# Performance work log

Hardware: AMD Instinct MI355X
Metric: run time of the kernel (lower is better)

Reference implementation:

```python
import jax, jax.numpy as jnp
import numpy as np

B, T, W, H, F = 256, 128, 32, 512, 1024


def setup_inputs() -> dict:
    key = jax.random.key(0)
    ks = jax.random.split(key, 8)
    s = 0.05
    return {
        "inputs": jax.random.normal(ks[0], (B, T, 2), jnp.float32),
        "Wk": jax.random.normal(ks[1], (2, 4 * H), jnp.float32) * s,
        "Wr": jax.random.normal(ks[2], (H, 4 * H), jnp.float32) * s,
        "b": jnp.zeros((4 * H,), jnp.float32),
        "Ww": jax.random.normal(ks[3], (H, 2), jnp.float32) * s,
        "bw": jnp.zeros((2,), jnp.float32),
        "Wc": jax.random.normal(ks[4], (2, H), jnp.float32) * s,
        "bc": jnp.zeros((H,), jnp.float32),
        "Wcc": jax.random.normal(ks[5], (W * H, F), jnp.float32) * s,
        "bcc": jnp.zeros((F,), jnp.float32),
        "Wp": jax.random.normal(ks[6], (F, 2), jnp.float32) * s,
        "bp": jnp.zeros((2,), jnp.float32),
        "Wco": jax.random.normal(ks[7], (F, 1), jnp.float32) * s,
        "bco": jnp.zeros((1,), jnp.float32),
    }


def _cell(x, h, c, Wk, Wr, b):
    # Keras LSTMCell: gate order i, f, g(candidate), o; sigmoid recurrent act, tanh act.
    z = x @ Wk + h @ Wr + b
    i, f, g, o = jnp.split(z, 4, axis=-1)
    c = jax.nn.sigmoid(f) * c + jax.nn.sigmoid(i) * jnp.tanh(g)
    h = jax.nn.sigmoid(o) * jnp.tanh(c)
    return h, c


def reference(inputs, Wk, Wr, b, Ww, bw, Wc, bc, Wcc, bcc, Wp, bp, Wco, bco):
    # Masking(-1.0) is a no-op for Gaussian inputs; dropout is identity at inference.
    warm_seq = jnp.swapaxes(inputs[:, W:], 0, 1)  # [T-W, B, 2]
    h0 = jnp.zeros((inputs.shape[0], H), inputs.dtype)
    c0 = jnp.zeros_like(h0)

    def warm_step(carry, x):
        h, c = carry
        h, c = _cell(x, h, c, Wk, Wr, b)
        return (h, c), None

    (h, c), _ = jax.lax.scan(warm_step, (h0, c0), warm_seq)
    warm_out = h  # warm_up_lstm_output, [B, H]
    pred0 = h @ Ww + bw  # dense_warm (linear activation), [B, 2]

    def dec_step(carry, _):
        h, c, pred = carry
        h, c = _cell(pred, h, c, Wk, Wr, b)
        pred = h @ Ww + bw
        return (h, c, pred), pred

    n_dec = T - W - 1  # range(1, time - warm_up_length)
    _, preds_rest = jax.lax.scan(dec_step, (h, c, pred0), None, length=n_dec)
    predictions = jnp.concatenate([pred0[None], preds_rest], axis=0)  # [T-W, B, 2]
    predictions = jnp.swapaxes(predictions, 0, 1)  # [B, T-W, 2]

    cand = jax.nn.relu(inputs[:, : W - 1] @ Wc + bc)  # [B, W-1, H]
    cand = cand.reshape(cand.shape[0], -1)  # flatten -> [B, (W-1)*H]
    cat = jnp.concatenate([warm_out, cand], axis=1)  # [B, W*H]
    ct = jax.nn.relu(cat @ Wcc + bcc)  # dense_concat, [B, F]
    candidate_prob = jax.nn.sigmoid(ct @ Wp + bp)  # [B, 2]
    candidate_cost = ct @ Wco + bco  # [B, 1]
    return predictions, candidate_cost, candidate_prob, inputs
```

## Files before the change

### kernel.cpp

```cpp
#include <hip/hip_runtime.h>
#include <hip/hip_bf16.h>
#include <stdint.h>

#define B_    256
#define T_    128
#define W_    32
#define H_    512
#define G4_   2048
#define TW_   96
#define STEPS_ 191
#define TEAMS 16
#define MEMBERS 16
#define ROWS  16
#define HC    32

typedef __attribute__((ext_vector_type(8))) short short8;
typedef __attribute__((ext_vector_type(4))) float f32x4;
typedef __attribute__((ext_vector_type(4))) uint32_t u32x4;

__device__ __forceinline__ unsigned short f2bf(float f) {
  uint32_t u = __float_as_uint(f);
  u += 0x7fffu + ((u >> 16) & 1u);
  return (unsigned short)(u >> 16);
}
__device__ __forceinline__ float sigm(float x) { return 1.f / (1.f + __expf(-x)); }
__device__ __forceinline__ float tanh_(float x) { return 1.f - 2.f / (1.f + __expf(2.f * x)); }

#define LOAD_CF(p)      __hip_atomic_load((p), __ATOMIC_RELAXED, __HIP_MEMORY_SCOPE_AGENT)
#define LOAD_CI(p)      __hip_atomic_load((p), __ATOMIC_RELAXED, __HIP_MEMORY_SCOPE_AGENT)
#define ARRIVE(p)       __hip_atomic_fetch_add((p), 1, __ATOMIC_RELAXED, __HIP_MEMORY_SCOPE_AGENT)

__device__ __forceinline__ u32x4 ld16c(const void* p) {
  u32x4 v;
  asm volatile("global_load_dwordx4 %0, %1, off sc0 sc1"
               : "=&v"(v) : "v"(p) : "memory");
  return v;
}
__device__ __forceinline__ void st16c(void* p, u32x4 v) {
  asm volatile("global_store_dwordx4 %0, %1, off sc0 sc1" :: "v"(p), "v"(v) : "memory");
}
__device__ __forceinline__ void stf16c(void* p, f32x4 v) {
  asm volatile("global_store_dwordx4 %0, %1, off sc0 sc1" :: "v"(p), "v"(v) : "memory");
}

__global__ __launch_bounds__(256, 1) void lstm_kernel(
    const float* __restrict__ inputs, const float* __restrict__ Wk,
    const float* __restrict__ Wr, const float* __restrict__ bias,
    const float* __restrict__ Ww, const float* __restrict__ bw,
    unsigned short* __restrict__ h0buf, unsigned short* __restrict__ h1buf,
    float* __restrict__ pp0, float* __restrict__ pp1,
    unsigned short* __restrict__ warm, int* __restrict__ flags,
    float* __restrict__ out_pred)
{
  const int team = blockIdx.x & 15;
  const int member = blockIdx.x >> 4;
  const int rbase = team * ROWS;
  const int hbase = member * HC;
  const int tid = threadIdx.x;
  const int wave = tid >> 6;
  const int lane = tid & 63;
  const int l4 = lane >> 4, l16 = lane & 15;

  __shared__ unsigned short h_lds[ROWS][H_];
  __shared__ float x_all[TW_][ROWS][2];
  __shared__ float x_lds[ROWS][2];
  __shared__ float pp_lds[4][ROWS][2];
  __shared__ alignas(16) unsigned short h_out[ROWS][HC];

  for (int i = tid; i < TW_*ROWS*2; i += 256) {
    int tt = i >> 5, row = (i >> 1) & 15, c = i & 1;
    x_all[tt][row][c] = inputs[(size_t)(rbase+row)*(T_*2) + (W_+tt)*2 + c];
  }

  const int gateL = l16 & 3, hclL = l16 >> 2;
  short8 afrag[2][16];
  float bbv[2][4], wk0v[2][4], wk1v[2][4], wwv[2][2];
#pragma unroll
  for (int a = 0; a < 2; a++) {
    const int gcA = gateL*H_ + hbase + wave*8 + a*4 + hclL;
#pragma unroll
    for (int ks = 0; ks < 16; ks++) {
      const float* wp = Wr + (size_t)(ks*32 + l4*8) * G4_ + gcA;
#pragma unroll
      for (int j = 0; j < 8; j++) afrag[a][ks][j] = (short)f2bf(wp[(size_t)j * G4_]);
    }
    const int colA = hbase + wave*8 + a*4 + l4;
#pragma unroll
    for (int j = 0; j < 4; j++) {
      int gcj = j*H_ + colA;
      bbv[a][j] = bias[gcj]; wk0v[a][j] = Wk[gcj]; wk1v[a][j] = Wk[G4_ + gcj];
    }
    wwv[a][0] = Ww[2*colA]; wwv[a][1] = Ww[2*colA + 1];
  }
  const float bwc0 = bw[0], bwc1 = bw[1];
  float creg[2] = {0.f, 0.f};
  __syncthreads();

  int* ctr = flags + team * 16;
  const int srow = tid >> 4, sg = tid & 15;

  for (int t = 0; t < STEPS_; t++) {
    const unsigned short* hprev = (t & 1) ? h1buf : h0buf;
    unsigned short* hnext = (t & 1) ? h0buf : h1buf;
    const float* ppprev = (t & 1) ? pp1 : pp0;
    float* ppnext = (t & 1) ? pp0 : pp1;

    const bool dox = (t >= TW_) && (tid < 32);
    float vals[MEMBERS];
    if (dox) {
      int row = tid >> 1, c = tid & 1;
      const float* pps = ppprev + (size_t)team*MEMBERS*32 + row*2 + c;
#pragma unroll
      for (int m = 0; m < MEMBERS; m++) vals[m] = LOAD_CF(pps + m*32);
    }
    u32x4 q[4];
    {
      const unsigned short* srcb = hprev + (size_t)(rbase+srow)*H_ + sg*8;
#pragma unroll
      for (int i = 0; i < 4; i++) q[i] = ld16c(srcb + i*128);
    }
    asm volatile("s_waitcnt vmcnt(0)" ::: "memory");
    __builtin_amdgcn_sched_barrier(0);
#pragma unroll
    for (int i = 0; i < 4; i++)
      *(u32x4*)&h_lds[srow][((sg + 16*i) ^ (srow & 7)) * 8] = q[i];
    if (dox) {
      int row = tid >> 1, c = tid & 1;
      float s = c ? bwc1 : bwc0;
#pragma unroll
      for (int m = 0; m < MEMBERS; m++) s += vals[m];
      x_lds[row][c] = s;
      if (member == 0)
        out_pred[((size_t)(rbase+row)*96 + (t - TW_))*2 + c] = s;
    }
    __syncthreads();

    f32x4 acc[2];
    const float* xsrc = (t < TW_) ? &x_all[t][0][0] : &x_lds[0][0];
    {
      float x0 = xsrc[2*l16], x1 = xsrc[2*l16 + 1];
#pragma unroll
      for (int a = 0; a < 2; a++)
#pragma unroll
        for (int j = 0; j < 4; j++)
          acc[a][j] = bbv[a][j] + wk0v[a][j]*x0 + wk1v[a][j]*x1;
    }
#pragma unroll
    for (int ks = 0; ks < 16; ks++) {
      int pg = ((ks*4 + l4) ^ (l16 & 7)) * 8;
      short8 b0 = *(const short8*)&h_lds[l16][pg];
      acc[0] = __builtin_amdgcn_mfma_f32_16x16x32_bf16(afrag[0][ks], b0, acc[0], 0,0,0);
      acc[1] = __builtin_amdgcn_mfma_f32_16x16x32_bf16(afrag[1][ks], b0, acc[1], 0,0,0);
    }

    float pp0v = 0.f, pp1v = 0.f;
#pragma unroll
    for (int a = 0; a < 2; a++) {
      float zi = acc[a][0], zf = acc[a][1], zg = acc[a][2], zo = acc[a][3];
      float cn = sigm(zf)*creg[a] + sigm(zi)*tanh_(zg);
      float hn = sigm(zo)*tanh_(cn);
      creg[a] = cn;
      pp0v += hn * wwv[a][0];
      pp1v += hn * wwv[a][1];
      h_out[l16][wave*8 + a*4 + l4] = f2bf(hn);
    }
    if (t >= TW_ - 1) {
      pp0v += __shfl_xor(pp0v, 16); pp0v += __shfl_xor(pp0v, 32);
      pp1v += __shfl_xor(pp1v, 16); pp1v += __shfl_xor(pp1v, 32);
      if (l4 == 0) {
        pp_lds[wave][l16][0] = pp0v;
        pp_lds[wave][l16][1] = pp1v;
      }
    }
    __syncthreads();

    if (tid < 64) {
      int row = tid >> 2, qd = tid & 3;
      u32x4 v = *(const u32x4*)&h_out[row][qd*8];
      st16c(hnext + (size_t)(rbase+row)*H_ + hbase + qd*8, v);
      if (t == TW_ - 1)
        *(u32x4*)(warm + (size_t)(rbase+row)*H_ + hbase + qd*8) = v;
    }
    if (t >= TW_ - 1 && tid < 8) {
      f32x4 pv;
#pragma unroll
      for (int j = 0; j < 4; j++) {
        int idx = tid*4 + j, row = idx >> 1, c = idx & 1;
        pv[j] = pp_lds[0][row][c] + pp_lds[1][row][c]
              + pp_lds[2][row][c] + pp_lds[3][row][c];
      }
      stf16c(ppnext + (size_t)(team*MEMBERS + member)*32 + tid*4, pv);
    }

    asm volatile("s_waitcnt vmcnt(0)" ::: "memory");
    __syncthreads();
    if (tid == 0) {
      ARRIVE(ctr);
      int need = MEMBERS * (t + 1);
      while (LOAD_CI(ctr) < need) {}
    }
    __syncthreads();
  }

  if (member == 0 && tid < 32) {
    int row = tid >> 1, c = tid & 1;
    const float* pps = pp1 + (size_t)team*MEMBERS*32 + row*2 + c;
    float s = c ? bwc1 : bwc0;
#pragma unroll
    for (int m = 0; m < MEMBERS; m++) s += LOAD_CF(pps + m*32);
    out_pred[((size_t)(rbase+row)*96 + 95)*2 + c] = s;
  }
}

__global__ __launch_bounds__(256, 1) void gemm_kernel(
    const float* __restrict__ inputs, const float* __restrict__ Wc,
    const float* __restrict__ bc, const float* __restrict__ Wcc,
    float* __restrict__ partialT)
{
  __shared__ float wc0[512], wc1[512], bcl[512];
  __shared__ float xin[256][10];

  const int tid = threadIdx.x;
  const int wave = tid >> 6, lane = tid & 63;
  const int l4 = lane >> 4, l16 = lane & 15;
  const int nc = blockIdx.x & 31, kc = blockIdx.x >> 5;
  const int koff = (kc == 0) ? 0 : kc*2048 - 512;
  const int nks  = (kc == 0) ? 48 : 64;
  const int w0 = koff >> 9;
  const int nw = (kc == 0) ? 3 : 5;

  for (int i = tid; i < 512; i += 256) {
    wc0[i] = Wc[i]; wc1[i] = Wc[512 + i]; bcl[i] = bc[i];
  }
  for (int i = tid; i < 256*nw*2; i += 256) {
    int row = i / (nw*2), r = i - row*(nw*2);
    xin[row][r] = inputs[(size_t)row*(T_*2) + w0*2 + r];
  }
  __syncthreads();

  const int nhalf = wave & 1, bhalf = wave >> 1;
  const int nrow = nc*32 + nhalf*16 + l16;
  f32x4 zero = {0.f,0.f,0.f,0.f};
  f32x4 acc[8];
#pragma unroll
  for (int i = 0; i < 8; i++) acc[i] = zero;

  for (int ks = 0; ks < nks; ks++) {
    const int kkl = koff + ks*32 + l4*8;
    const float* wp = Wcc + (size_t)(512 + kkl) * 1024 + nrow;
    short8 af;
#pragma unroll
    for (int j = 0; j < 8; j++) af[j] = (short)f2bf(wp[(size_t)j * 1024]);
    const int w = kkl >> 9, hc = kkl & 511;
    const int wi = (w - w0)*2;
    float c0[8], c1[8], cb[8];
#pragma unroll
    for (int j = 0; j < 8; j++) {
      c0[j] = wc0[hc+j]; c1[j] = wc1[hc+j]; cb[j] = bcl[hc+j];
    }
#pragma unroll
    for (int bt = 0; bt < 8; bt++) {
      int row = bhalf*128 + bt*16 + l16;
      float x0 = xin[row][wi], x1 = xin[row][wi+1];
      short8 bf;
#pragma unroll
      for (int j = 0; j < 8; j++) {
        float v = fmaf(x0, c0[j], fmaf(x1, c1[j], cb[j]));
        bf[j] = (short)f2bf(fmaxf(v, 0.f));
      }
      acc[bt] = __builtin_amdgcn_mfma_f32_16x16x32_bf16(af, bf, acc[bt], 0,0,0);
    }
  }
  float* pp = partialT + (size_t)kc*262144
            + (size_t)(nc*32 + nhalf*16 + l4*4)*256 + bhalf*128 + l16;
#pragma unroll
  for (int bt = 0; bt < 8; bt++)
#pragma unroll
    for (int r = 0; r < 4; r++)
      pp[(size_t)r*256 + bt*16] = acc[bt][r];
}

__global__ __launch_bounds__(256, 1) void gemm0_kernel(
    const unsigned short* __restrict__ warm, const float* __restrict__ Wcc,
    float* __restrict__ partial8)
{
  const int nc = blockIdx.x;
  const int tid = threadIdx.x;
  const int w = tid >> 6, lane = tid & 63;
  const int l4 = lane >> 4, l16 = lane & 15;

  f32x4 zero = {0.f,0.f,0.f,0.f};
  f32x4 acc[16];
#pragma unroll
  for (int i = 0; i < 16; i++) acc[i] = zero;

  const int nrow = nc*64 + w*16 + l16;
  for (int ks = 0; ks < 16; ks++) {
    const float* wp = Wcc + (size_t)(ks*32 + l4*8) * 1024 + nrow;
    short8 af;
#pragma unroll
    for (int j = 0; j < 8; j++) af[j] = (short)f2bf(wp[(size_t)j * 1024]);
    const unsigned short* cp = warm + ks*32 + l4*8;
#pragma unroll
    for (int bt = 0; bt < 16; bt++) {
      short8 bf = *(const short8*)(cp + (size_t)(bt*16 + l16) * 512);
      acc[bt] = __builtin_amdgcn_mfma_f32_16x16x32_bf16(af, bf, acc[bt], 0,0,0);
    }
  }
  float* pp = partial8 + (size_t)(nc*64 + w*16 + l4*4)*256 + l16;
#pragma unroll
  for (int bt = 0; bt < 16; bt++)
#pragma unroll
    for (int r = 0; r < 4; r++)
      pp[(size_t)r*256 + bt*16] = acc[bt][r];
}

__global__ void reduce_kernel(const float* __restrict__ partialT,
                              const float* __restrict__ partial8,
                              const float* __restrict__ bcc, float* __restrict__ ctT,
                              const float* __restrict__ inputs, float* __restrict__ out)
{
  int e = blockIdx.x * 256 + threadIdx.x;
  int n = e >> 8;
  float s = bcc[n] + partial8[e];
#pragma unroll
  for (int p = 0; p < 8; p++) s += partialT[(size_t)p*262144 + e];
  ctT[e] = fmaxf(s, 0.f);
  if (e < 65536) out[49920 + e] = inputs[e];
}

__global__ void head_kernel(const float* __restrict__ ctT, const float* __restrict__ Wp,
                            const float* __restrict__ bp, const float* __restrict__ Wco,
                            const float* __restrict__ bco, float* __restrict__ out)
{
  int b = blockIdx.x;
  int lane = threadIdx.x;
  float p0 = 0.f, p1 = 0.f, pc = 0.f;
#pragma unroll
  for (int i = 0; i < 16; i++) {
    int n = i*64 + lane;
    float c = ctT[(size_t)n*256 + b];
    p0 += c * Wp[2*n]; p1 += c * Wp[2*n+1]; pc += c * Wco[n];
  }
  for (int m = 1; m < 64; m <<= 1) {
    p0 += __shfl_xor(p0, m); p1 += __shfl_xor(p1, m); pc += __shfl_xor(pc, m);
  }
  if (lane == 0) {
    out[49152 + b]       = pc + bco[0];
    out[49408 + 2*b]     = 1.f / (1.f + __expf(-(p0 + bp[0])));
    out[49408 + 2*b + 1] = 1.f / (1.f + __expf(-(p1 + bp[1])));
  }
}

extern "C" void kernel_launch(void* const* d_in, const int* in_sizes, int n_in,
                              void* d_out, int out_size, void* d_ws, size_t ws_size,
                              hipStream_t stream) {
  const float* inputs = (const float*)d_in[0];
  const float* Wk   = (const float*)d_in[1];
  const float* Wr   = (const float*)d_in[2];
  const float* bias = (const float*)d_in[3];
  const float* Ww   = (const float*)d_in[4];
  const float* bw   = (const float*)d_in[5];
  const float* Wc   = (const float*)d_in[6];
  const float* bc   = (const float*)d_in[7];
  const float* Wcc  = (const float*)d_in[8];
  const float* bcc  = (const float*)d_in[9];
  const float* Wp   = (const float*)d_in[10];
  const float* bp   = (const float*)d_in[11];
  const float* Wco  = (const float*)d_in[12];
  const float* bco  = (const float*)d_in[13];
  float* out = (float*)d_out;
  char* ws = (char*)d_ws;

  unsigned short* h0   = (unsigned short*)(ws);
  int*            flags= (int*)(ws + 0x40000);
  unsigned short* h1   = (unsigned short*)(ws + 0x42000);
  unsigned short* warm = (unsigned short*)(ws + 0x82000);
  float*          pp0  = (float*)(ws + 0xC2000);
  float*          pp1  = (float*)(ws + 0xCA000);
  float*          partial8 = (float*)(ws + 0xD2000);
  float*          partialT = (float*)(ws + 0x8C2000);
  float*          ctT  = (float*)(ws + 0x10C2000);

  hipMemsetAsync(d_ws, 0, 0x42000, stream);

  lstm_kernel<<<TEAMS*MEMBERS, 256, 0, stream>>>(inputs, Wk, Wr, bias, Ww, bw,
                                                 h0, h1, pp0, pp1, warm, flags, out);
  gemm_kernel<<<256, 256, 0, stream>>>(inputs, Wc, bc, Wcc, partialT);
  gemm0_kernel<<<16, 256, 0, stream>>>(warm, Wcc, partial8);
  reduce_kernel<<<1024, 256, 0, stream>>>(partialT, partial8, bcc, ctT, inputs, out);
  head_kernel<<<256, 64, 0, stream>>>(ctT, Wp, bp, Wco, bco, out);
}
```

Measured before the change: 713.7 us.

## Fuse candidate GEMM into persistent LSTM kernel, overlapping with barrier waits

Removes the separate candidate-dense GEMM launch and spreads its k-steps across the LSTM's 191 recurrent steps, running one MFMA k-slice every third step between signalling arrival and spinning on the team barrier. The Wcc operand for the next slice is prefetched into registers so its latency is hidden behind the recurrence. The intent is to use idle time spent waiting at the inter-block barrier for GEMM work and to drop one kernel launch. In exchange the LSTM kernel takes on extra registers and LDS, and the added work on each step may lengthen the serial critical path.

```diff
diff --git a/kernel.cpp b/kernel.cpp
--- a/kernel.cpp
+++ b/kernel.cpp
@@ -47,10 +47,12 @@
     const float* __restrict__ inputs, const float* __restrict__ Wk,
     const float* __restrict__ Wr, const float* __restrict__ bias,
     const float* __restrict__ Ww, const float* __restrict__ bw,
+    const float* __restrict__ Wc, const float* __restrict__ bc,
+    const float* __restrict__ Wcc,
     unsigned short* __restrict__ h0buf, unsigned short* __restrict__ h1buf,
     float* __restrict__ pp0, float* __restrict__ pp1,
     unsigned short* __restrict__ warm, int* __restrict__ flags,
-    float* __restrict__ out_pred)
+    float* __restrict__ partialT, float* __restrict__ out_pred)
 {
   const int team = blockIdx.x & 15;
   const int member = blockIdx.x >> 4;
@@ -66,11 +68,25 @@
   __shared__ float x_lds[ROWS][2];
   __shared__ float pp_lds[4][ROWS][2];
   __shared__ alignas(16) unsigned short h_out[ROWS][HC];
+  __shared__ float wc0[512], wc1[512], bcl[512];
+  __shared__ float xin[256][10];
+
+  const int kc = blockIdx.x >> 5, gnc = blockIdx.x & 31;
+  const int koff = (kc == 0) ? 0 : kc*2048 - 512;
+  const int nks  = (kc == 0) ? 48 : 64;
+  const int gw0 = koff >> 9;
 
   for (int i = tid; i < TW_*ROWS*2; i += 256) {
     int tt = i >> 5, row = (i >> 1) & 15, c = i & 1;
     x_all[tt][row][c] = inputs[(size_t)(rbase+row)*(T_*2) + (W_+tt)*2 + c];
   }
+  for (int i = tid; i < 512; i += 256) {
+    wc0[i] = Wc[i]; wc1[i] = Wc[512 + i]; bcl[i] = bc[i];
+  }
+  for (int i = tid; i < 2560; i += 256) {
+    int row = i / 10, r = i - row*10;
+    xin[row][r] = inputs[(size_t)row*(T_*2) + gw0*2 + r];
+  }
 
   const int gateL = l16 & 3, hclL = l16 >> 2;
   short8 afrag[2][16];
@@ -94,6 +110,19 @@
   }
   const float bwc0 = bw[0], bwc1 = bw[1];
   float creg[2] = {0.f, 0.f};
+
+  const int nhalf = wave & 1, bhalf = wave >> 1;
+  const int gnrow = gnc*32 + nhalf*16 + l16;
+  f32x4 gacc[8];
+#pragma unroll
+  for (int i = 0; i < 8; i++) gacc[i] = (f32x4){0.f,0.f,0.f,0.f};
+  float fn[8];
+  {
+    const float* wp = Wcc + (size_t)(512 + koff + l4*8) * 1024 + gnrow;
+#pragma unroll
+    for (int j = 0; j < 8; j++) fn[j] = wp[(size_t)j * 1024];
+  }
+  int gq = 0, gphase = 0;
   __syncthreads();
 
   int* ctr = flags + team * 16;
@@ -194,8 +223,42 @@
 
     asm volatile("s_waitcnt vmcnt(0)" ::: "memory");
     __syncthreads();
+    if (tid == 0) ARRIVE(ctr);
+
+    if (gphase == 0 && gq < nks) {
+      const int kkl = koff + gq*32 + l4*8;
+      short8 af;
+#pragma unroll
+      for (int j = 0; j < 8; j++) af[j] = (short)f2bf(fn[j]);
+      if (gq + 1 < nks) {
+        const float* wp = Wcc + (size_t)(512 + kkl + 32) * 1024 + gnrow;
+#pragma unroll
+        for (int j = 0; j < 8; j++) fn[j] = wp[(size_t)j * 1024];
+      }
+      const int w = kkl >> 9, hc = kkl & 511;
+      const int wi = (w - gw0)*2;
+      float c0[8], c1[8], cb[8];
+#pragma unroll
+      for (int j = 0; j < 8; j++) {
+        c0[j] = wc0[hc+j]; c1[j] = wc1[hc+j]; cb[j] = bcl[hc+j];
+      }
+#pragma unroll
+      for (int bt = 0; bt < 8; bt++) {
+        int row = bhalf*128 + bt*16 + l16;
+        float x0 = xin[row][wi], x1 = xin[row][wi+1];
+        short8 bf;
+#pragma unroll
+        for (int j = 0; j < 8; j++) {
+          float v = fmaf(x0, c0[j], fmaf(x1, c1[j], cb[j]));
+          bf[j] = (short)f2bf(fmaxf(v, 0.f));
+        }
+        gacc[bt] = __builtin_amdgcn_mfma_f32_16x16x32_bf16(af, bf, gacc[bt], 0,0,0);
+      }
+      gq++;
+    }
+    gphase = (gphase == 2) ? 0 : gphase + 1;
+
     if (tid == 0) {
-      ARRIVE(ctr);
       int need = MEMBERS * (t + 1);
       while (LOAD_CI(ctr) < need) {}
     }
@@ -210,74 +273,16 @@
     for (int m = 0; m < MEMBERS; m++) s += LOAD_CF(pps + m*32);
     out_pred[((size_t)(rbase+row)*96 + 95)*2 + c] = s;
   }
-}
-
-__global__ __launch_bounds__(256, 1) void gemm_kernel(
-    const float* __restrict__ inputs, const float* __restrict__ Wc,
-    const float* __restrict__ bc, const float* __restrict__ Wcc,
-    float* __restrict__ partialT)
-{
-  __shared__ float wc0[512], wc1[512], bcl[512];
-  __shared__ float xin[256][10];
-
-  const int tid = threadIdx.x;
-  const int wave = tid >> 6, lane = tid & 63;
-  const int l4 = lane >> 4, l16 = lane & 15;
-  const int nc = blockIdx.x & 31, kc = blockIdx.x >> 5;
-  const int koff = (kc == 0) ? 0 : kc*2048 - 512;
-  const int nks  = (kc == 0) ? 48 : 64;
-  const int w0 = koff >> 9;
-  const int nw = (kc == 0) ? 3 : 5;
-
-  for (int i = tid; i < 512; i += 256) {
-    wc0[i] = Wc[i]; wc1[i] = Wc[512 + i]; bcl[i] = bc[i];
-  }
-  for (int i = tid; i < 256*nw*2; i += 256) {
-    int row = i / (nw*2), r = i - row*(nw*2);
-    xin[row][r] = inputs[(size_t)row*(T_*2) + w0*2 + r];
-  }
-  __syncthreads();
-
-  const int nhalf = wave & 1, bhalf = wave >> 1;
-  const int nrow = nc*32 + nhalf*16 + l16;
-  f32x4 zero = {0.f,0.f,0.f,0.f};
-  f32x4 acc[8];
-#pragma unroll
-  for (int i = 0; i < 8; i++) acc[i] = zero;
-
-  for (int ks = 0; ks < nks; ks++) {
-    const int kkl = koff + ks*32 + l4*8;
-    const float* wp = Wcc + (size_t)(512 + kkl) * 1024 + nrow;
-    short8 af;
-#pragma unroll
-    for (int j = 0; j < 8; j++) af[j] = (short)f2bf(wp[(size_t)j * 1024]);
-    const int w = kkl >> 9, hc = kkl & 511;
-    const int wi = (w - w0)*2;
-    float c0[8], c1[8], cb[8];
-#pragma unroll
-    for (int j = 0; j < 8; j++) {
-      c0[j] = wc0[hc+j]; c1[j] = wc1[hc+j]; cb[j] = bcl[hc+j];
-    }
-#pragma unroll
-    for (int bt = 0; bt < 8; bt++) {
-      int row = bhalf*128 + bt*16 + l16;
-      float x0 = xin[row][wi], x1 = xin[row][wi+1];
-      short8 bf;
-#pragma unroll
-      for (int j = 0; j < 8; j++) {
-        float v = fmaf(x0, c0[j], fmaf(x1, c1[j], cb[j]));
-        bf[j] = (short)f2bf(fmaxf(v, 0.f));
-      }
-      acc[bt] = __builtin_amdgcn_mfma_f32_16x16x32_bf16(af, bf, acc[bt], 0,0,0);
-    }
-  }
-  float* pp = partialT + (size_t)kc*262144
-            + (size_t)(nc*32 + nhalf*16 + l4*4)*256 + bhalf*128 + l16;
-#pragma unroll
-  for (int bt = 0; bt < 8; bt++)
-#pragma unroll
-    for (int r = 0; r < 4; r++)
-      pp[(size_t)r*256 + bt*16] = acc[bt][r];
+
+  {
+    float* pp = partialT + (size_t)kc*262144
+              + (size_t)(gnc*32 + nhalf*16 + l4*4)*256 + bhalf*128 + l16;
+#pragma unroll
+    for (int bt = 0; bt < 8; bt++)
+#pragma unroll
+      for (int r = 0; r < 4; r++)
+        pp[(size_t)r*256 + bt*16] = gacc[bt][r];
+  }
 }
 
 __global__ __launch_bounds__(256, 1) void gemm0_kernel(
@@ -385,8 +390,9 @@
   hipMemsetAsync(d_ws, 0, 0x42000, stream);
 
   lstm_kernel<<<TEAMS*MEMBERS, 256, 0, stream>>>(inputs, Wk, Wr, bias, Ww, bw,
-                                                 h0, h1, pp0, pp1, warm, flags, out);
-  gemm_kernel<<<256, 256, 0, stream>>>(inputs, Wc, bc, Wcc, partialT);
+                                                 Wc, bc, Wcc,
+                                                 h0, h1, pp0, pp1, warm, flags,
+                                                 partialT, out);
   gemm0_kernel<<<16, 256, 0, stream>>>(warm, Wcc, partial8);
   reduce_kernel<<<1024, 256, 0, stream>>>(partialT, partial8, bcc, ctT, inputs, out);
   head_kernel<<<256, 64, 0, stream>>>(ctT, Wp, bp, Wco, bco, out);
```

Result: faster. 652.9 us (-8.5%).
